# Optimization experiments

Measured on AMD Instinct MI355X. Metric: run time of the kernel, lower is better.

Reference implementation:

```python
import jax, jax.numpy as jnp
import numpy as np

B, S, D, H = 2, 2048, 1024, 16
HD = D // H

def setup_inputs() -> dict:
    key = jax.random.key(0)
    ks = jax.random.split(key, 6)
    X = jax.random.normal(ks[0], (B, S, D), dtype=jnp.float32)
    mask = jax.random.randint(ks[1], (B, 1, S, S), 0, 2, dtype=jnp.int32)
    scale = 1.0 / np.sqrt(D)
    Wq = jax.random.normal(ks[2], (D, D), dtype=jnp.float32) * scale
    Wk = jax.random.normal(ks[3], (D, D), dtype=jnp.float32) * scale
    Wv = jax.random.normal(ks[4], (D, D), dtype=jnp.float32) * scale
    Wo = jax.random.normal(ks[5], (D, D), dtype=jnp.float32) * scale
    return {"X": X, "mask": mask, "Wq": Wq, "Wk": Wk, "Wv": Wv, "Wo": Wo}

def reference(X, mask, Wq, Wk, Wv, Wo):
    b, s, d = X.shape
    # torch nn.Linear(bias=False): y = x @ W.T, W is [out, in]
    def split_heads(Y):
        return Y.reshape(b, s, H, HD).transpose(0, 2, 1, 3)  # [b,h,s,hd]
    Q = split_heads(X @ Wq.T)
    K = split_heads(X @ Wk.T)
    V = split_heads(X @ Wv.T)
    scores = jnp.einsum('bhqd,bhkd->bhqk', Q, K) / jnp.sqrt(jnp.float32(HD))
    # Faithful to original: masked positions filled with -1e-09 (sic)
    scores = jnp.where(mask == 0, jnp.float32(-1e-09), scores)
    # dropout p=0.0 -> identity (applied to scores pre-softmax in original)
    weights = jax.nn.softmax(scores, axis=-1)
    out = jnp.einsum('bhqk,bhkd->bhqd', weights, V)  # [b,h,s,hd]
    out = out.transpose(0, 2, 1, 3).reshape(b, s, d)
    return out @ Wo.T
```

## Files before the change

### kernel.cpp

```cpp
#include <hip/hip_runtime.h>
#include <hip/hip_bf16.h>

using short8  = __attribute__((ext_vector_type(8))) short;
using short4v = __attribute__((ext_vector_type(4))) short;
using f32x4   = __attribute__((ext_vector_type(4))) float;

#if __has_builtin(__builtin_amdgcn_exp2f)
#define EXP2(x) __builtin_amdgcn_exp2f(x)
#else
#define EXP2(x) __expf(0.6931471805599453f*(x))
#endif

__device__ __forceinline__ unsigned short f2bf(float x){
  union { float f; unsigned u; } c; c.f = x;
  unsigned u = c.u + 0x7FFFu + ((c.u >> 16) & 1u);
  return (unsigned short)(u >> 16);
}

__device__ __forceinline__ unsigned pack_bf16_rn(float a, float b){
  __hip_bfloat162 t = __float22bfloat162_rn(make_float2(a, b));
  unsigned u; __builtin_memcpy(&u, &t, 4);
  return u;
}

__global__ __launch_bounds__(256) void prep(const float* __restrict__ X, const int* __restrict__ Mk,
                                            const float* __restrict__ Wq, const float* __restrict__ Wk,
                                            const float* __restrict__ Wv, const float* __restrict__ Wo,
                                            unsigned short* __restrict__ Xb, unsigned short* __restrict__ Wqkv,
                                            unsigned short* __restrict__ Wob, unsigned char* __restrict__ M8)
{
  const int bid = blockIdx.x, tid = threadIdx.x;
  if (bid < 8192){
    const float* src; unsigned short* dst; float scale; int i;
    if (bid < 4096)      { src = X;  dst = Xb;             scale = 1.0f;          i = bid*1024 + tid*4; }
    else if (bid < 5120) { src = Wq; dst = Wqkv;           scale = 0.18033688f;   i = (bid-4096)*1024 + tid*4; }
    else if (bid < 6144) { src = Wk; dst = Wqkv + 1048576; scale = 1.0f;          i = (bid-5120)*1024 + tid*4; }
    else if (bid < 7168) { src = Wv; dst = Wqkv + 2097152; scale = 1.0f;          i = (bid-6144)*1024 + tid*4; }
    else                 { src = Wo; dst = Wob;            scale = 1.0f;          i = (bid-7168)*1024 + tid*4; }
    float4 v = *(const float4*)(src + i);
    ushort4 o;
    o.x = f2bf(v.x * scale); o.y = f2bf(v.y * scale);
    o.z = f2bf(v.z * scale); o.w = f2bf(v.w * scale);
    *(ushort4*)(dst + i) = o;
  } else {
    int i = (bid - 8192)*1024 + tid*4;
    int4 v = *(const int4*)(Mk + i);
    unsigned out = (v.x ? 1u : 0u) | ((v.y ? 1u : 0u) << 8) |
                   ((v.z ? 1u : 0u) << 16) | ((v.w ? 1u : 0u) << 24);
    *(unsigned*)(M8 + i) = out;
  }
}

__device__ __forceinline__ void stage16(const unsigned short* g, unsigned short* l){
  __builtin_amdgcn_global_load_lds(
      (const __attribute__((address_space(1))) void*)g,
      (__attribute__((address_space(3))) void*)l, 16, 0, 0);
}

__global__ __launch_bounds__(256) void gemm_qkv(const unsigned short* __restrict__ A,
                                                const unsigned short* __restrict__ B,
                                                unsigned short* __restrict__ C,
                                                unsigned short* __restrict__ Vg)
{
  __shared__ unsigned short As[128*32];
  __shared__ unsigned short Bs[128*32];
  const int tid = threadIdx.x;
  const int wave = tid >> 6, lane = tid & 63, l16 = lane & 15, quad = lane >> 4;
  const int id = blockIdx.x, xcd = id & 7, m = id >> 3;
  const int bm = (m / 3) * 128, bn = (xcd * 3 + (m % 3)) * 128;
  const int wm = (wave >> 1) * 64, wn = (wave & 1) * 64;
  const int K = 1024;

  f32x4 acc[4][4] = {};
  for (int k0 = 0; k0 < K; k0 += 32){
    #pragma unroll
    for (int c = 0; c < 2; c++){
      int idx = c * 256 + tid;
      int row = idx >> 2, g = (idx & 3) * 8;
      stage16(A + (size_t)(bm + row) * K + k0 + g, &As[idx * 8]);
      stage16(B + (size_t)(bn + row) * K + k0 + g, &Bs[idx * 8]);
    }
    __syncthreads();
    short8 af[4], bf[4];
    #pragma unroll
    for (int i = 0; i < 4; i++) af[i] = *(const short8*)&As[(wm + i*16 + l16)*32 + quad*8];
    #pragma unroll
    for (int j = 0; j < 4; j++) bf[j] = *(const short8*)&Bs[(wn + j*16 + l16)*32 + quad*8];
    #pragma unroll
    for (int i = 0; i < 4; i++)
      #pragma unroll
      for (int j = 0; j < 4; j++)
        acc[i][j] = __builtin_amdgcn_mfma_f32_16x16x32_bf16(af[i], bf[j], acc[i][j], 0, 0, 0);
    __syncthreads();
  }

  if (bn < 2048){
    #pragma unroll
    for (int i = 0; i < 4; i++){
      int mrow = bm + wm + i*16 + quad*4;
      #pragma unroll
      for (int j = 0; j < 4; j++){
        int ncol = bn + wn + j*16 + l16;
        #pragma unroll
        for (int r = 0; r < 4; r++)
          C[(size_t)(mrow + r) * 3072 + ncol] = f2bf(acc[i][j][r]);
      }
    }
  } else {
    #pragma unroll
    for (int i = 0; i < 4; i++){
      int srow = bm + wm + i*16 + quad*4;
      int b = srow >> 11, s = srow & 2047;
      #pragma unroll
      for (int j = 0; j < 4; j++){
        int c = bn - 2048 + wn + j*16 + l16;
        int h = c >> 6, d = c & 63;
        ushort4 o;
        o.x = f2bf(acc[i][j][0]); o.y = f2bf(acc[i][j][1]);
        o.z = f2bf(acc[i][j][2]); o.w = f2bf(acc[i][j][3]);
        *(ushort4*)&Vg[((size_t)(b*16 + h)*64 + d) * 2048 + s] = o;
      }
    }
  }
}

__global__ __launch_bounds__(256) void gemm_out(const unsigned short* __restrict__ A,
                                                const unsigned short* __restrict__ B,
                                                float* __restrict__ Cf)
{
  __shared__ unsigned short As[128*32];
  __shared__ unsigned short Bs[64*32];
  const int tid = threadIdx.x;
  const int wave = tid >> 6, lane = tid & 63, l16 = lane & 15, quad = lane >> 4;
  const int id = blockIdx.x, xcd = id & 7, m = id >> 3;
  const int bm = (m >> 1) * 128, bn = (xcd * 2 + (m & 1)) * 64;
  const int wm = (wave >> 1) * 64, wn = (wave & 1) * 32;
  const int K = 1024, N = 1024;

  f32x4 acc[4][2] = {};
  for (int k0 = 0; k0 < K; k0 += 32){
    #pragma unroll
    for (int c = 0; c < 2; c++){
      int idx = c * 256 + tid;
      int row = idx >> 2, g = (idx & 3) * 8;
      stage16(A + (size_t)(bm + row) * K + k0 + g, &As[idx * 8]);
    }
    stage16(B + (size_t)(bn + (tid >> 2)) * K + k0 + (tid & 3) * 8, &Bs[tid * 8]);
    __syncthreads();
    short8 af[4], bf[2];
    #pragma unroll
    for (int i = 0; i < 4; i++) af[i] = *(const short8*)&As[(wm + i*16 + l16)*32 + quad*8];
    #pragma unroll
    for (int j = 0; j < 2; j++) bf[j] = *(const short8*)&Bs[(wn + j*16 + l16)*32 + quad*8];
    #pragma unroll
    for (int i = 0; i < 4; i++)
      #pragma unroll
      for (int j = 0; j < 2; j++)
        acc[i][j] = __builtin_amdgcn_mfma_f32_16x16x32_bf16(af[i], bf[j], acc[i][j], 0, 0, 0);
    __syncthreads();
  }
  #pragma unroll
  for (int i = 0; i < 4; i++){
    int mrow = bm + wm + i*16 + quad*4;
    #pragma unroll
    for (int j = 0; j < 2; j++){
      int ncol = bn + wn + j*16 + l16;
      #pragma unroll
      for (int r = 0; r < 4; r++)
        Cf[(size_t)(mrow + r) * N + ncol] = acc[i][j][r];
    }
  }
}

__global__ __launch_bounds__(256, 3) void attn(const unsigned short* __restrict__ QKV,
                                               const unsigned short* __restrict__ Vg,
                                               const unsigned char* __restrict__ mask8,
                                               unsigned short* __restrict__ O)
{
  __shared__ char smem[40960];
  unsigned short* Ks = (unsigned short*)smem;
  unsigned short* Vt = (unsigned short*)(smem + 16384);
  unsigned short* Ps = (unsigned short*)(smem + 32768);
  float* lsums = (float*)smem;

  const int tid = threadIdx.x, wave = tid >> 6, lane = tid & 63;
  const int l16 = lane & 15, quad = lane >> 4;
  const int id = blockIdx.x;
  const int xcd = id & 7, m = id >> 3;
  const int bh = xcd * 4 + (m >> 5);
  const int qblk = (m & 31) * 64;
  const int b = bh >> 4, h = bh & 15;
  const unsigned short* Qg  = QKV + (size_t)b * 2048 * 3072 + h * 64;
  const unsigned short* Kg  = Qg + 1024;
  const unsigned short* Vgb = Vg + (size_t)bh * 64 * 2048;
  const unsigned char*  mbase = mask8 + (size_t)b * 2048 * 2048;

  short8 qf[4][2];
  #pragma unroll
  for (int nt = 0; nt < 4; nt++)
    #pragma unroll
    for (int ks = 0; ks < 2; ks++)
      qf[nt][ks] = *(const short8*)(Qg + (size_t)(qblk + nt*16 + l16) * 3072 + ks*32 + quad*8);

  f32x4 oacc[4] = {};
  float plsum[4] = {0.f, 0.f, 0.f, 0.f};
  const int sw = l16 & 7;

  #pragma unroll
  for (int it = 0; it < 2; it++){
    int s = it * 256 + tid;
    int row = s >> 3, bg = (s & 7) ^ (row & 7);
    stage16(Kg + (size_t)row * 3072 + bg * 8, Ks + s * 8);
    stage16(Vgb + (size_t)row * 2048 + bg * 8, Vt + s * 8);
  }

  for (int c = 0; c < 32; c++){
    const int j0 = c * 64;
    const int buf = (c & 1) * 4096;
    __syncthreads();

    if (c < 31){
      const int nj = j0 + 64, nbuf = ((c + 1) & 1) * 4096;
      #pragma unroll
      for (int it = 0; it < 2; it++){
        int s = it * 256 + tid;
        int row = s >> 3, bg = (s & 7) ^ (row & 7);
        stage16(Kg + (size_t)(nj + row) * 3072 + bg * 8, Ks + nbuf + s * 8);
        stage16(Vgb + (size_t)row * 2048 + nj + bg * 8, Vt + nbuf + s * 8);
      }
    }

    unsigned md[4];
    #pragma unroll
    for (int nt = 0; nt < 4; nt++)
      md[nt] = *(const unsigned*)(mbase + (size_t)(qblk + nt*16 + l16) * 2048 + j0 + wave*16 + quad*4);

    short8 kf0 = *(const short8*)&Ks[buf + (wave*16 + l16) * 64 + ((0 + quad) ^ sw) * 8];
    short8 kf1 = *(const short8*)&Ks[buf + (wave*16 + l16) * 64 + ((4 + quad) ^ sw) * 8];
    #pragma unroll
    for (int nt = 0; nt < 4; nt++){
      f32x4 a = {0.f, 0.f, 0.f, 0.f};
      a = __builtin_amdgcn_mfma_f32_16x16x32_bf16(kf0, qf[nt][0], a, 0, 0, 0);
      a = __builtin_amdgcn_mfma_f32_16x16x32_bf16(kf1, qf[nt][1], a, 0, 0, 0);
      float p0 = EXP2(a[0] * (float)( md[nt]        & 255u));
      float p1 = EXP2(a[1] * (float)((md[nt] >>  8) & 255u));
      float p2 = EXP2(a[2] * (float)((md[nt] >> 16) & 255u));
      float p3 = EXP2(a[3] * (float)( md[nt] >> 24        ));
      plsum[nt] += (p0 + p1) + (p2 + p3);
      uint2 st; st.x = pack_bf16_rn(p0, p1); st.y = pack_bf16_rn(p2, p3);
      *(uint2*)&Ps[(nt*16 + l16) * 64 + ((wave*2 + (quad >> 1)) ^ sw) * 8 + (quad & 1) * 4] = st;
    }

    __asm__ volatile("s_waitcnt lgkmcnt(0)" ::: "memory");
    __builtin_amdgcn_s_barrier();
    __asm__ volatile("" ::: "memory");

    #pragma unroll
    for (int kk = 0; kk < 4; kk++){
      int pb = (kk*2 + (quad >> 1)) ^ sw;
      short4v a2 = *(const short4v*)&Vt[buf + (wave*16 + l16) * 64 + pb * 8 + (quad & 1) * 4];
      #pragma unroll
      for (int nt = 0; nt < 4; nt++){
        short4v b2 = *(const short4v*)&Ps[(nt*16 + l16) * 64 + pb * 8 + (quad & 1) * 4];
        oacc[nt] = __builtin_amdgcn_mfma_f32_16x16x16bf16_1k(a2, b2, oacc[nt], 0, 0, 0);
      }
    }
  }

  float lw[4];
  #pragma unroll
  for (int nt = 0; nt < 4; nt++){
    float v = plsum[nt];
    v += __shfl_xor(v, 16);
    v += __shfl_xor(v, 32);
    lw[nt] = v;
  }
  __syncthreads();
  if (quad == 0){
    #pragma unroll
    for (int nt = 0; nt < 4; nt++) lsums[(nt*16 + l16) * 4 + wave] = lw[nt];
  }
  __syncthreads();
  float linv[4];
  #pragma unroll
  for (int nt = 0; nt < 4; nt++){
    f32x4 ls = *(const f32x4*)&lsums[(nt*16 + l16) * 4];
    linv[nt] = 1.0f / (ls[0] + ls[1] + ls[2] + ls[3]);
  }
  #pragma unroll
  for (int nt = 0; nt < 4; nt++){
    f32x4 t = oacc[nt];
    unsigned u0 = pack_bf16_rn(t[0] * linv[nt], t[1] * linv[nt]);
    unsigned u1 = pack_bf16_rn(t[2] * linv[nt], t[3] * linv[nt]);
    uint2 st; st.x = u0; st.y = u1;
    *(uint2*)&O[(size_t)(b*2048 + qblk + nt*16 + l16) * 1024 + h*64 + wave*16 + quad*4] = st;
  }
}

extern "C" void kernel_launch(void* const* d_in, const int* in_sizes, int n_in,
                              void* d_out, int out_size, void* d_ws, size_t ws_size,
                              hipStream_t stream)
{
  const float* X  = (const float*)d_in[0];
  const int*   Mk = (const int*)d_in[1];
  const float* Wq = (const float*)d_in[2];
  const float* Wk = (const float*)d_in[3];
  const float* Wv = (const float*)d_in[4];
  const float* Wo = (const float*)d_in[5];
  float* out = (float*)d_out;

  char* ws = (char*)d_ws;
  unsigned short* Xb   = (unsigned short*)(ws + 0);
  unsigned short* Wqkv = (unsigned short*)(ws + 8388608);
  unsigned short* Wob  = (unsigned short*)(ws + 14680064);
  unsigned short* QKV  = (unsigned short*)(ws + 16777216);
  unsigned short* Ob   = (unsigned short*)(ws + 41943040);
  unsigned char*  M8   = (unsigned char*) (ws + 50331648);
  unsigned short* Vg   = (unsigned short*)(ws + 58720256);

  prep<<<16384, 256, 0, stream>>>(X, Mk, Wq, Wk, Wv, Wo, Xb, Wqkv, Wob, M8);
  gemm_qkv<<<768, 256, 0, stream>>>(Xb, Wqkv, QKV, Vg);
  attn<<<1024, 256, 0, stream>>>(QKV, Vg, M8, Ob);
  gemm_out<<<512, 256, 0, stream>>>(Ob, Wob, out);
}
```

Baseline: 260.2 us.

## Pack mask to bits, prefetch mask words, and use 32-wide MFMA for PV

The prep kernel now compresses the int32 mask into 1-bit-per-element words using wave ballots, writing 8x less mask data than the previous byte mask. The attention kernel reads 16-bit mask words per row, prefetches the next chunk's mask into registers, and selects exp2(score) or 1.0 per element instead of multiplying the score by the mask byte. The PV product switches from 16x16x16 to 16x16x32 bf16 MFMA with 8-element fragment loads, and s_setprio is raised around the MFMA blocks. This adds select instructions and a bit-layout dependency between the ballot ordering and the per-lane bit extraction.

```diff
diff --git a/kernel.cpp b/kernel.cpp
--- a/kernel.cpp
+++ b/kernel.cpp
@@ -2,7 +2,6 @@
 #include <hip/hip_bf16.h>
 
 using short8  = __attribute__((ext_vector_type(8))) short;
-using short4v = __attribute__((ext_vector_type(4))) short;
 using f32x4   = __attribute__((ext_vector_type(4))) float;
 
 #if __has_builtin(__builtin_amdgcn_exp2f)
@@ -27,7 +26,7 @@
                                             const float* __restrict__ Wq, const float* __restrict__ Wk,
                                             const float* __restrict__ Wv, const float* __restrict__ Wo,
                                             unsigned short* __restrict__ Xb, unsigned short* __restrict__ Wqkv,
-                                            unsigned short* __restrict__ Wob, unsigned char* __restrict__ M8)
+                                            unsigned short* __restrict__ Wob, unsigned long long* __restrict__ Mbits)
 {
   const int bid = blockIdx.x, tid = threadIdx.x;
   if (bid < 8192){
@@ -43,11 +42,16 @@
     o.z = f2bf(v.z * scale); o.w = f2bf(v.w * scale);
     *(ushort4*)(dst + i) = o;
   } else {
-    int i = (bid - 8192)*1024 + tid*4;
-    int4 v = *(const int4*)(Mk + i);
-    unsigned out = (v.x ? 1u : 0u) | ((v.y ? 1u : 0u) << 8) |
-                   ((v.z ? 1u : 0u) << 16) | ((v.w ? 1u : 0u) << 24);
-    *(unsigned*)(M8 + i) = out;
+    int row = bid - 8192;
+    const int* src = Mk + (size_t)row * 2048;
+    unsigned long long* dst = Mbits + (size_t)row * 32;
+    int w = tid >> 6, l = tid & 63;
+    #pragma unroll
+    for (int p = 0; p < 8; p++){
+      int v = src[w*512 + p*64 + l];
+      unsigned long long bm = __ballot(v != 0);
+      if (l == 0) dst[w*8 + p] = bm;
+    }
   }
 }
 
@@ -174,7 +178,7 @@
 
 __global__ __launch_bounds__(256, 3) void attn(const unsigned short* __restrict__ QKV,
                                                const unsigned short* __restrict__ Vg,
-                                               const unsigned char* __restrict__ mask8,
+                                               const unsigned short* __restrict__ mask16,
                                                unsigned short* __restrict__ O)
 {
   __shared__ char smem[40960];
@@ -193,7 +197,11 @@
   const unsigned short* Qg  = QKV + (size_t)b * 2048 * 3072 + h * 64;
   const unsigned short* Kg  = Qg + 1024;
   const unsigned short* Vgb = Vg + (size_t)bh * 64 * 2048;
-  const unsigned char*  mbase = mask8 + (size_t)b * 2048 * 2048;
+
+  const unsigned short* mp[4];
+  #pragma unroll
+  for (int nt = 0; nt < 4; nt++)
+    mp[nt] = mask16 + (size_t)(b*2048 + qblk + nt*16 + l16) * 128 + wave;
 
   short8 qf[4][2];
   #pragma unroll
@@ -213,6 +221,9 @@
     stage16(Kg + (size_t)row * 3072 + bg * 8, Ks + s * 8);
     stage16(Vgb + (size_t)row * 2048 + bg * 8, Vt + s * 8);
   }
+  unsigned mcur[4], mnxt[4] = {0u, 0u, 0u, 0u};
+  #pragma unroll
+  for (int nt = 0; nt < 4; nt++) mcur[nt] = mp[nt][0];
 
   for (int c = 0; c < 32; c++){
     const int j0 = c * 64;
@@ -228,24 +239,28 @@
         stage16(Kg + (size_t)(nj + row) * 3072 + bg * 8, Ks + nbuf + s * 8);
         stage16(Vgb + (size_t)row * 2048 + nj + bg * 8, Vt + nbuf + s * 8);
       }
-    }
-
-    unsigned md[4];
-    #pragma unroll
-    for (int nt = 0; nt < 4; nt++)
-      md[nt] = *(const unsigned*)(mbase + (size_t)(qblk + nt*16 + l16) * 2048 + j0 + wave*16 + quad*4);
+      #pragma unroll
+      for (int nt = 0; nt < 4; nt++) mnxt[nt] = mp[nt][(c + 1) * 4];
+    }
 
     short8 kf0 = *(const short8*)&Ks[buf + (wave*16 + l16) * 64 + ((0 + quad) ^ sw) * 8];
     short8 kf1 = *(const short8*)&Ks[buf + (wave*16 + l16) * 64 + ((4 + quad) ^ sw) * 8];
     #pragma unroll
     for (int nt = 0; nt < 4; nt++){
       f32x4 a = {0.f, 0.f, 0.f, 0.f};
+      __builtin_amdgcn_s_setprio(1);
       a = __builtin_amdgcn_mfma_f32_16x16x32_bf16(kf0, qf[nt][0], a, 0, 0, 0);
       a = __builtin_amdgcn_mfma_f32_16x16x32_bf16(kf1, qf[nt][1], a, 0, 0, 0);
-      float p0 = EXP2(a[0] * (float)( md[nt]        & 255u));
-      float p1 = EXP2(a[1] * (float)((md[nt] >>  8) & 255u));
-      float p2 = EXP2(a[2] * (float)((md[nt] >> 16) & 255u));
-      float p3 = EXP2(a[3] * (float)( md[nt] >> 24        ));
+      __builtin_amdgcn_s_setprio(0);
+      float p0 = EXP2(a[0]);
+      float p1 = EXP2(a[1]);
+      float p2 = EXP2(a[2]);
+      float p3 = EXP2(a[3]);
+      unsigned mq = mcur[nt] >> (quad << 2);
+      p0 = (mq & 1u) ? p0 : 1.0f;
+      p1 = (mq & 2u) ? p1 : 1.0f;
+      p2 = (mq & 4u) ? p2 : 1.0f;
+      p3 = (mq & 8u) ? p3 : 1.0f;
       plsum[nt] += (p0 + p1) + (p2 + p3);
       uint2 st; st.x = pack_bf16_rn(p0, p1); st.y = pack_bf16_rn(p2, p3);
       *(uint2*)&Ps[(nt*16 + l16) * 64 + ((wave*2 + (quad >> 1)) ^ sw) * 8 + (quad & 1) * 4] = st;
@@ -253,18 +268,24 @@
 
     __asm__ volatile("s_waitcnt lgkmcnt(0)" ::: "memory");
     __builtin_amdgcn_s_barrier();
-    __asm__ volatile("" ::: "memory");
-
-    #pragma unroll
-    for (int kk = 0; kk < 4; kk++){
-      int pb = (kk*2 + (quad >> 1)) ^ sw;
-      short4v a2 = *(const short4v*)&Vt[buf + (wave*16 + l16) * 64 + pb * 8 + (quad & 1) * 4];
-      #pragma unroll
-      for (int nt = 0; nt < 4; nt++){
-        short4v b2 = *(const short4v*)&Ps[(nt*16 + l16) * 64 + pb * 8 + (quad & 1) * 4];
-        oacc[nt] = __builtin_amdgcn_mfma_f32_16x16x16bf16_1k(a2, b2, oacc[nt], 0, 0, 0);
-      }
-    }
+    __builtin_amdgcn_sched_barrier(0);
+
+    #pragma unroll
+    for (int kk = 0; kk < 2; kk++){
+      short8 vfrag = *(const short8*)&Vt[buf + (wave*16 + l16) * 64 + ((kk*4 + quad) ^ sw) * 8];
+      short8 pf[4];
+      #pragma unroll
+      for (int nt = 0; nt < 4; nt++)
+        pf[nt] = *(const short8*)&Ps[(nt*16 + l16) * 64 + ((kk*4 + quad) ^ sw) * 8];
+      __builtin_amdgcn_s_setprio(1);
+      #pragma unroll
+      for (int nt = 0; nt < 4; nt++)
+        oacc[nt] = __builtin_amdgcn_mfma_f32_16x16x32_bf16(vfrag, pf[nt], oacc[nt], 0, 0, 0);
+      __builtin_amdgcn_s_setprio(0);
+    }
+
+    #pragma unroll
+    for (int nt = 0; nt < 4; nt++) mcur[nt] = mnxt[nt];
   }
 
   float lw[4];
@@ -315,11 +336,11 @@
   unsigned short* Wob  = (unsigned short*)(ws + 14680064);
   unsigned short* QKV  = (unsigned short*)(ws + 16777216);
   unsigned short* Ob   = (unsigned short*)(ws + 41943040);
-  unsigned char*  M8   = (unsigned char*) (ws + 50331648);
+  unsigned long long* Mb = (unsigned long long*)(ws + 50331648);
   unsigned short* Vg   = (unsigned short*)(ws + 58720256);
 
-  prep<<<16384, 256, 0, stream>>>(X, Mk, Wq, Wk, Wv, Wo, Xb, Wqkv, Wob, M8);
+  prep<<<12288, 256, 0, stream>>>(X, Mk, Wq, Wk, Wv, Wo, Xb, Wqkv, Wob, Mb);
   gemm_qkv<<<768, 256, 0, stream>>>(Xb, Wqkv, QKV, Vg);
-  attn<<<1024, 256, 0, stream>>>(QKV, Vg, M8, Ob);
+  attn<<<1024, 256, 0, stream>>>(QKV, Vg, (const unsigned short*)Mb, Ob);
   gemm_out<<<512, 256, 0, stream>>>(Ob, Wob, out);
 }
```

Result: slower. 268.4 us (+3.1%).
